# Performance work log

Hardware: AMD Instinct MI355X
Metric: run time of the kernel (lower is better)

Reference implementation:

```python
import jax, jax.numpy as jnp
import numpy as np

N_SETS, N_POINTS, D_FEAT = 8, 4096, 16
K = 16


def setup_inputs() -> dict:
    key = jax.random.key(0)
    x = jax.random.normal(key, (N_SETS, N_POINTS, D_FEAT), dtype=jnp.float32)
    return {"x": x, "k": K}


def reference(x, k):
    """Faithful kNN-graph construction.

    x: (N, M, D) point sets. Returns (src, dst) flattened edge lists with
    per-sample node-ID offsets (node j of set i -> global id i*M + j), plus
    the top-k squared distances (the selection values).
    """
    n_samples, n_points, _ = x.shape
    # pairwise squared distance: ||xi||^2 + ||xj||^2 - 2 xi.xj  -> (N, M, M)
    x2s = jnp.sum(x * x, axis=-1, keepdims=True)
    dist = x2s + jnp.swapaxes(x2s, -1, -2) - 2.0 * jnp.einsum("nmd,npd->nmp", x, x)
    # k smallest distances per row (argtopk descending=False)
    neg_vals, k_indices = jax.lax.top_k(-dist, k)            # (N, M, k)
    topk_dist = -neg_vals
    per_sample_offset = (jnp.arange(n_samples, dtype=jnp.int32) * n_points)[:, None, None]
    dst = k_indices.astype(jnp.int32) + per_sample_offset     # neighbor ids
    src = jnp.broadcast_to(
        jnp.arange(n_points, dtype=jnp.int32)[None, :, None], k_indices.shape
    ) + per_sample_offset                                     # query ids
    return src.reshape(-1), dst.reshape(-1), topk_dist
```

## Files before the change

### kernel.cpp

```cpp
#include <hip/hip_runtime.h>

typedef unsigned long long u64;

#define NSETS 8
#define NPTS  4096
#define DF    16
#define KNN   16
#define QPB   64
#define NCH   8
#define BLK   (QPB * NCH)
#define TILE  512
#define NTILE (NPTS / TILE)
#define SLICE (TILE / NCH)
#define NEDGE (NSETS * NPTS * KNN)

#define RES      10
#define FLUSH_AT 7
#define GRP      4

#define FEAT_B   (TILE * DF * 4)
#define NRM_B    (TILE * 4)
#define RESV_OFF (FEAT_B + NRM_B)
#define SMEM_B   (RESV_OFF + RES * BLK * 8)
#define MPAD     17

__device__ __forceinline__ unsigned flip_f(float d) {
    unsigned b = __float_as_uint(d);
    return (b & 0x80000000u) ? ~b : (b | 0x80000000u);
}
__device__ __forceinline__ float unflip_f(unsigned u) {
    unsigned b = (u & 0x80000000u) ? (u ^ 0x80000000u) : ~u;
    return __uint_as_float(b);
}

#define CEB(i, j) { u64 _a = B[i], _b = B[j]; bool _c = _b < _a; \
                    B[i] = _c ? _b : _a; B[j] = _c ? _a : _b; }
#define CEL(i, j) { u64 _a = Lk[i], _b = Lk[j]; bool _c = _b < _a; \
                    Lk[i] = _c ? _b : _a; Lk[j] = _c ? _a : _b; }
#define MERGE16() \
    CEL(0,8)  CEL(1,9)  CEL(2,10) CEL(3,11)  \
    CEL(4,12) CEL(5,13) CEL(6,14) CEL(7,15)  \
    CEL(0,4)  CEL(1,5)  CEL(2,6)  CEL(3,7)   \
    CEL(8,12) CEL(9,13) CEL(10,14) CEL(11,15) \
    CEL(0,2)  CEL(1,3)  CEL(4,6)  CEL(5,7)   \
    CEL(8,10) CEL(9,11) CEL(12,14) CEL(13,15) \
    CEL(0,1)  CEL(2,3)  CEL(4,5)  CEL(6,7)   \
    CEL(8,9)  CEL(10,11) CEL(12,13) CEL(14,15)

__global__ __launch_bounds__(BLK) void knn_kernel(const float* __restrict__ x,
                                                  float* __restrict__ out) {
    __shared__ float tau_sh[QPB];
    __shared__ float tau2_sh[NCH * QPB];
    __shared__ __align__(16) char smem[SMEM_B];
    float4* feat4 = (float4*)smem;
    float*  nrm_t = (float*)(smem + FEAT_B);
    u64*    resv  = (u64*)(smem + RESV_OFF);
    float*          lds_d = (float*)smem;
    unsigned short* lds_i = (unsigned short*)(smem + BLK * MPAD * 4);

    const int t    = threadIdx.x;
    const int lane = t & 63;
    const int wv   = t >> 6;
    const int set  = blockIdx.x >> 6;
    const int q0   = (blockIdx.x & 63) * QPB;
    const int q    = q0 + lane;

    const float* xs = x + (size_t)set * NPTS * DF;

    if (t < QPB) tau_sh[t] = 3.0e38f;
    tau2_sh[t] = 3.0e38f;

    float qn[DF];
    float q2;
    {
        const float4* qp = (const float4*)(xs + (size_t)q * DF);
        float4 a = qp[0], b = qp[1], g = qp[2], d = qp[3];
        float r0 = __fadd_rn(__fmul_rn(a.x, a.x), __fmul_rn(g.x, g.x));
        float r1 = __fadd_rn(__fmul_rn(a.y, a.y), __fmul_rn(g.y, g.y));
        float r2 = __fadd_rn(__fmul_rn(a.z, a.z), __fmul_rn(g.z, g.z));
        float r3 = __fadd_rn(__fmul_rn(a.w, a.w), __fmul_rn(g.w, g.w));
        float r4 = __fadd_rn(__fmul_rn(b.x, b.x), __fmul_rn(d.x, d.x));
        float r5 = __fadd_rn(__fmul_rn(b.y, b.y), __fmul_rn(d.y, d.y));
        float r6 = __fadd_rn(__fmul_rn(b.z, b.z), __fmul_rn(d.z, d.z));
        float r7 = __fadd_rn(__fmul_rn(b.w, b.w), __fmul_rn(d.w, d.w));
        q2 = __fadd_rn(__fadd_rn(__fadd_rn(r0, r1), __fadd_rn(r2, r3)),
                       __fadd_rn(__fadd_rn(r4, r5), __fadd_rn(r6, r7)));
        qn[0]=a.x; qn[1]=a.y; qn[2]=a.z; qn[3]=a.w;
        qn[4]=b.x; qn[5]=b.y; qn[6]=b.z; qn[7]=b.w;
        qn[8]=g.x; qn[9]=g.y; qn[10]=g.z; qn[11]=g.w;
        qn[12]=d.x; qn[13]=d.y; qn[14]=d.z; qn[15]=d.w;
#pragma unroll
        for (int d2 = 0; d2 < DF; ++d2) qn[d2] = -2.0f * qn[d2];
    }

    const u64 SENT = ((u64)flip_f(3.0e38f) << 32) | 0xFFFFFFFFull;
    u64   Lk[KNN];
#pragma unroll
    for (int j = 0; j < KNN; ++j) Lk[j] = SENT;
    float tau_reg = 3.0e38f;
    int   cnt = 0;

    auto drain = [&]() {
        {
            u64 B[8];
#pragma unroll
            for (int e = 0; e < 8; ++e) {
                u64 v = resv[e * BLK + t];
                B[e] = (e < cnt) ? v : SENT;
            }
            CEB(0,1) CEB(2,3) CEB(4,5) CEB(6,7)
            CEB(0,2) CEB(1,3) CEB(4,6) CEB(5,7)
            CEB(1,2) CEB(5,6)
            CEB(0,4) CEB(1,5) CEB(2,6) CEB(3,7)
            CEB(2,4) CEB(3,5)
            CEB(1,2) CEB(3,4) CEB(5,6)
#pragma unroll
            for (int i = 0; i < 8; ++i) {
                u64 a = Lk[KNN - 1 - i], b = B[i];
                Lk[KNN - 1 - i] = (b < a) ? b : a;
            }
            MERGE16()
        }
        if (__any(cnt > 8)) {
            u64 c0 = resv[8 * BLK + t];
            u64 c1 = resv[9 * BLK + t];
            c0 = (8 < cnt) ? c0 : SENT;
            c1 = (9 < cnt) ? c1 : SENT;
            { u64 a = c0, b = c1; bool c = b < a; c0 = c ? b : a; c1 = c ? a : b; }
            { u64 a = Lk[15]; Lk[15] = (c0 < a) ? c0 : a; }
            { u64 a = Lk[14]; Lk[14] = (c1 < a) ? c1 : a; }
            MERGE16()
        }
        cnt = 0;
        const float kth = unflip_f((unsigned)(Lk[KNN - 1] >> 32));
        volatile float* t2 = (volatile float*)tau2_sh;
        t2[wv * QPB + lane] = unflip_f((unsigned)(Lk[1] >> 32));
        float gmax = t2[0 * QPB + lane];
#pragma unroll
        for (int j = 1; j < NCH; ++j) gmax = fmaxf(gmax, t2[j * QPB + lane]);
        const float kth2 = fminf(kth, gmax);
        tau_reg = kth2;
        volatile float* ts = (volatile float*)tau_sh;
        float cur = ts[lane];
        ts[lane] = fminf(cur, kth2);
    };

    for (int tile = 0; tile < NTILE; ++tile) {
        __syncthreads();
        {
            const int c = tile * TILE + t;
            const float4* p = (const float4*)(xs + (size_t)c * DF);
            float4 a = p[0], b = p[1], g = p[2], d = p[3];
            float r0 = __fadd_rn(__fmul_rn(a.x, a.x), __fmul_rn(g.x, g.x));
            float r1 = __fadd_rn(__fmul_rn(a.y, a.y), __fmul_rn(g.y, g.y));
            float r2 = __fadd_rn(__fmul_rn(a.z, a.z), __fmul_rn(g.z, g.z));
            float r3 = __fadd_rn(__fmul_rn(a.w, a.w), __fmul_rn(g.w, g.w));
            float r4 = __fadd_rn(__fmul_rn(b.x, b.x), __fmul_rn(d.x, d.x));
            float r5 = __fadd_rn(__fmul_rn(b.y, b.y), __fmul_rn(d.y, d.y));
            float r6 = __fadd_rn(__fmul_rn(b.z, b.z), __fmul_rn(d.z, d.z));
            float r7 = __fadd_rn(__fmul_rn(b.w, b.w), __fmul_rn(d.w, d.w));
            feat4[0 * TILE + t] = a;
            feat4[1 * TILE + t] = b;
            feat4[2 * TILE + t] = g;
            feat4[3 * TILE + t] = d;
            nrm_t[t] = __fadd_rn(
                __fadd_rn(__fadd_rn(r0, r1), __fadd_rn(r2, r3)),
                __fadd_rn(__fadd_rn(r4, r5), __fadd_rn(r6, r7)));
        }
        __syncthreads();

        const int lbase = wv * SLICE;
        const int gbase = tile * TILE + lbase;

        for (int g = 0; g < SLICE; g += GRP) {
            const float tsh = ((volatile float*)tau_sh)[lane];
            const float tau = fminf(tsh, tau_reg);
#pragma unroll
            for (int u = 0; u < GRP; ++u) {
                const int lc = lbase + g + u;
                float4 f0 = feat4[0 * TILE + lc];
                float4 f1 = feat4[1 * TILE + lc];
                float4 f2 = feat4[2 * TILE + lc];
                float4 f3 = feat4[3 * TILE + lc];
                const float nc = nrm_t[lc];
                float dot = 0.f;
                dot = fmaf(qn[0],  f0.x, dot); dot = fmaf(qn[1],  f0.y, dot);
                dot = fmaf(qn[2],  f0.z, dot); dot = fmaf(qn[3],  f0.w, dot);
                dot = fmaf(qn[4],  f1.x, dot); dot = fmaf(qn[5],  f1.y, dot);
                dot = fmaf(qn[6],  f1.z, dot); dot = fmaf(qn[7],  f1.w, dot);
                dot = fmaf(qn[8],  f2.x, dot); dot = fmaf(qn[9],  f2.y, dot);
                dot = fmaf(qn[10], f2.z, dot); dot = fmaf(qn[11], f2.w, dot);
                dot = fmaf(qn[12], f3.x, dot); dot = fmaf(qn[13], f3.y, dot);
                dot = fmaf(qn[14], f3.z, dot); dot = fmaf(qn[15], f3.w, dot);
                const float dist = __fadd_rn(__fadd_rn(q2, nc), dot);
                if (dist <= tau) {
                    resv[cnt * BLK + t] =
                        ((u64)flip_f(dist) << 32) | (unsigned)(gbase + g + u);
                    ++cnt;
                }
            }
            if (__any(cnt >= FLUSH_AT)) drain();
        }
    }
    if (__any(cnt > 0)) drain();

    __syncthreads();
#pragma unroll
    for (int j = 0; j < KNN; ++j) {
        lds_d[t * MPAD + j] = unflip_f((unsigned)(Lk[j] >> 32));
        lds_i[t * MPAD + j] = (unsigned short)(Lk[j] & 0xFFFFu);
    }
    __syncthreads();

    if (t < QPB) {
        const int l = t;
        float h[NCH];
        int   hi[NCH];
        int   p[NCH];
#pragma unroll
        for (int w2 = 0; w2 < NCH; ++w2) {
            p[w2]  = 0;
            h[w2]  = lds_d[(w2 * QPB + l) * MPAD];
            hi[w2] = (int)lds_i[(w2 * QPB + l) * MPAD];
        }

        const int    gq = set * NPTS + q0 + l;
        const size_t eb = (size_t)gq * KNN;
        float* osrc = out;
        float* odst = out + (size_t)NEDGE;
        float* odis = out + 2 * (size_t)NEDGE;
        const float srcf = (float)gq;

        for (int e = 0; e < KNN; ++e) {
            float best = h[0];
            int   bi   = hi[0];
            int   bw   = 0;
#pragma unroll
            for (int w2 = 1; w2 < NCH; ++w2) {
                const bool better = (h[w2] < best) ||
                                    (h[w2] == best && hi[w2] < bi);
                if (better) { best = h[w2]; bi = hi[w2]; bw = w2; }
            }

#pragma unroll
            for (int w2 = 0; w2 < NCH; ++w2) {
                if (bw == w2) {
                    ++p[w2];
                    if (p[w2] < KNN) {
                        h[w2]  = lds_d[(w2 * QPB + l) * MPAD + p[w2]];
                        hi[w2] = (int)lds_i[(w2 * QPB + l) * MPAD + p[w2]];
                    } else {
                        h[w2]  = 3.0e38f;
                        hi[w2] = 0x7FFFFFFF;
                    }
                }
            }

            osrc[eb + e] = srcf;
            odst[eb + e] = (float)(set * NPTS + bi);
            odis[eb + e] = best;
        }
    }
}

extern "C" void kernel_launch(void* const* d_in, const int* in_sizes, int n_in,
                              void* d_out, int out_size, void* d_ws, size_t ws_size,
                              hipStream_t stream) {
    (void)in_sizes; (void)n_in; (void)out_size; (void)d_ws; (void)ws_size;
    const float* x = (const float*)d_in[0];
    float* out = (float*)d_out;

    knn_kernel<<<NSETS * (NPTS / QPB), BLK, 0, stream>>>(x, out);
}
```

Baseline: 199.8 us.

## Interleave candidate pairs in LDS for packed FP32 FMA and branchless reservoir writes

Candidate points are staged in shared memory as interleaved pairs, so each query computes two distances at once with 2-wide vector FMAs. On this hardware these can map to packed FP32 instructions, roughly halving the dot-product instruction count. Candidate norms are stored as two partial sums and added at use time, which slightly changes rounding order. The reservoir is split into separate distance and index arrays and filled branchlessly: every candidate is written and the count advances only when it passes the threshold, which removes divergent branches at the cost of extra LDS stores.

```diff
diff --git a/kernel.cpp b/kernel.cpp
--- a/kernel.cpp
+++ b/kernel.cpp
@@ -1,6 +1,9 @@
 #include <hip/hip_runtime.h>
 
 typedef unsigned long long u64;
+typedef unsigned int u32;
+typedef float f2 __attribute__((ext_vector_type(2)));
+typedef float f4 __attribute__((ext_vector_type(4)));
 
 #define NSETS 8
 #define NPTS  4096
@@ -12,15 +15,17 @@
 #define TILE  512
 #define NTILE (NPTS / TILE)
 #define SLICE (TILE / NCH)
+#define PAIRS_W (SLICE / 2)
 #define NEDGE (NSETS * NPTS * KNN)
 
 #define RES      10
 #define FLUSH_AT 7
-#define GRP      4
-
-#define FEAT_B   (TILE * DF * 4)
-#define NRM_B    (TILE * 4)
-#define RESV_OFF (FEAT_B + NRM_B)
+#define GRP      2
+
+#define PF_B     (TILE * DF * 4)
+#define PRT_OFF  PF_B
+#define RESV_OFF (PF_B + 4096)
+#define RESI_OFF (RESV_OFF + RES * BLK * 4)
 #define SMEM_B   (RESV_OFF + RES * BLK * 8)
 #define MPAD     17
 
@@ -31,6 +36,16 @@
 __device__ __forceinline__ float unflip_f(unsigned u) {
     unsigned b = (u & 0x80000000u) ? (u ^ 0x80000000u) : ~u;
     return __uint_as_float(b);
+}
+
+__device__ __forceinline__ f2 sp2(float v) { f2 r = {v, v}; return r; }
+
+__device__ __forceinline__ f2 fma2(f2 a, f2 b, f2 c) {
+#if __has_builtin(__builtin_elementwise_fma)
+    return __builtin_elementwise_fma(a, b, c);
+#else
+    f2 r; r.x = fmaf(a.x, b.x, c.x); r.y = fmaf(a.y, b.y, c.y); return r;
+#endif
 }
 
 #define CEB(i, j) { u64 _a = B[i], _b = B[j]; bool _c = _b < _a; \
@@ -52,9 +67,10 @@
     __shared__ float tau_sh[QPB];
     __shared__ float tau2_sh[NCH * QPB];
     __shared__ __align__(16) char smem[SMEM_B];
-    float4* feat4 = (float4*)smem;
-    float*  nrm_t = (float*)(smem + FEAT_B);
-    u64*    resv  = (u64*)(smem + RESV_OFF);
+    f4*    pf   = (f4*)smem;
+    f2*    prt  = (f2*)(smem + PRT_OFF);
+    float* resd = (float*)(smem + RESV_OFF);
+    u32*   resi = (u32*)(smem + RESI_OFF);
     float*          lds_d = (float*)smem;
     unsigned short* lds_i = (unsigned short*)(smem + BLK * MPAD * 4);
 
@@ -92,6 +108,7 @@
 #pragma unroll
         for (int d2 = 0; d2 < DF; ++d2) qn[d2] = -2.0f * qn[d2];
     }
+    const f2 q22 = sp2(q2);
 
     const u64 SENT = ((u64)flip_f(3.0e38f) << 32) | 0xFFFFFFFFull;
     u64   Lk[KNN];
@@ -105,8 +122,10 @@
             u64 B[8];
 #pragma unroll
             for (int e = 0; e < 8; ++e) {
-                u64 v = resv[e * BLK + t];
-                B[e] = (e < cnt) ? v : SENT;
+                float de = resd[e * BLK + t];
+                u32   ie = resi[e * BLK + t];
+                u64 key = ((u64)flip_f(de) << 32) | ie;
+                B[e] = (e < cnt) ? key : SENT;
             }
             CEB(0,1) CEB(2,3) CEB(4,5) CEB(6,7)
             CEB(0,2) CEB(1,3) CEB(4,6) CEB(5,7)
@@ -122,8 +141,10 @@
             MERGE16()
         }
         if (__any(cnt > 8)) {
-            u64 c0 = resv[8 * BLK + t];
-            u64 c1 = resv[9 * BLK + t];
+            float d8 = resd[8 * BLK + t], d9 = resd[9 * BLK + t];
+            u32   i8 = resi[8 * BLK + t], i9 = resi[9 * BLK + t];
+            u64 c0 = ((u64)flip_f(d8) << 32) | i8;
+            u64 c1 = ((u64)flip_f(d9) << 32) | i9;
             c0 = (8 < cnt) ? c0 : SENT;
             c1 = (9 < cnt) ? c1 : SENT;
             { u64 a = c0, b = c1; bool c = b < a; c0 = c ? b : a; c1 = c ? a : b; }
@@ -148,56 +169,78 @@
     for (int tile = 0; tile < NTILE; ++tile) {
         __syncthreads();
         {
-            const int c = tile * TILE + t;
-            const float4* p = (const float4*)(xs + (size_t)c * DF);
-            float4 a = p[0], b = p[1], g = p[2], d = p[3];
-            float r0 = __fadd_rn(__fmul_rn(a.x, a.x), __fmul_rn(g.x, g.x));
-            float r1 = __fadd_rn(__fmul_rn(a.y, a.y), __fmul_rn(g.y, g.y));
-            float r2 = __fadd_rn(__fmul_rn(a.z, a.z), __fmul_rn(g.z, g.z));
-            float r3 = __fadd_rn(__fmul_rn(a.w, a.w), __fmul_rn(g.w, g.w));
-            float r4 = __fadd_rn(__fmul_rn(b.x, b.x), __fmul_rn(d.x, d.x));
-            float r5 = __fadd_rn(__fmul_rn(b.y, b.y), __fmul_rn(d.y, d.y));
-            float r6 = __fadd_rn(__fmul_rn(b.z, b.z), __fmul_rn(d.z, d.z));
-            float r7 = __fadd_rn(__fmul_rn(b.w, b.w), __fmul_rn(d.w, d.w));
-            feat4[0 * TILE + t] = a;
-            feat4[1 * TILE + t] = b;
-            feat4[2 * TILE + t] = g;
-            feat4[3 * TILE + t] = d;
-            nrm_t[t] = __fadd_rn(
-                __fadd_rn(__fadd_rn(r0, r1), __fadd_rn(r2, r3)),
-                __fadd_rn(__fadd_rn(r4, r5), __fadd_rn(r6, r7)));
+            const int p  = t & 255;
+            const int hf = t >> 8;
+            const float4* rowA =
+                (const float4*)(xs + (size_t)(tile * TILE + 2 * p) * DF);
+            float4 a0 = rowA[hf];
+            float4 a2 = rowA[hf + 2];
+            float4 b0 = rowA[hf + 4];
+            float4 b2 = rowA[hf + 6];
+            const int jb0 = 2 * hf;
+            const int jb2 = 4 + 2 * hf;
+            pf[(jb0 + 0) * 256 + p] = (f4){a0.x, b0.x, a0.y, b0.y};
+            pf[(jb0 + 1) * 256 + p] = (f4){a0.z, b0.z, a0.w, b0.w};
+            pf[(jb2 + 0) * 256 + p] = (f4){a2.x, b2.x, a2.y, b2.y};
+            pf[(jb2 + 1) * 256 + p] = (f4){a2.z, b2.z, a2.w, b2.w};
+            float ra0 = __fadd_rn(__fmul_rn(a0.x, a0.x), __fmul_rn(a2.x, a2.x));
+            float ra1 = __fadd_rn(__fmul_rn(a0.y, a0.y), __fmul_rn(a2.y, a2.y));
+            float ra2 = __fadd_rn(__fmul_rn(a0.z, a0.z), __fmul_rn(a2.z, a2.z));
+            float ra3 = __fadd_rn(__fmul_rn(a0.w, a0.w), __fmul_rn(a2.w, a2.w));
+            float rb0 = __fadd_rn(__fmul_rn(b0.x, b0.x), __fmul_rn(b2.x, b2.x));
+            float rb1 = __fadd_rn(__fmul_rn(b0.y, b0.y), __fmul_rn(b2.y, b2.y));
+            float rb2 = __fadd_rn(__fmul_rn(b0.z, b0.z), __fmul_rn(b2.z, b2.z));
+            float rb3 = __fadd_rn(__fmul_rn(b0.w, b0.w), __fmul_rn(b2.w, b2.w));
+            f2 s;
+            s.x = __fadd_rn(__fadd_rn(ra0, ra1), __fadd_rn(ra2, ra3));
+            s.y = __fadd_rn(__fadd_rn(rb0, rb1), __fadd_rn(rb2, rb3));
+            prt[hf * 256 + p] = s;
         }
         __syncthreads();
 
-        const int lbase = wv * SLICE;
-        const int gbase = tile * TILE + lbase;
-
-        for (int g = 0; g < SLICE; g += GRP) {
+        const int pb = wv * PAIRS_W;
+
+        for (int g = 0; g < PAIRS_W; g += GRP) {
             const float tsh = ((volatile float*)tau_sh)[lane];
             const float tau = fminf(tsh, tau_reg);
 #pragma unroll
             for (int u = 0; u < GRP; ++u) {
-                const int lc = lbase + g + u;
-                float4 f0 = feat4[0 * TILE + lc];
-                float4 f1 = feat4[1 * TILE + lc];
-                float4 f2 = feat4[2 * TILE + lc];
-                float4 f3 = feat4[3 * TILE + lc];
-                const float nc = nrm_t[lc];
-                float dot = 0.f;
-                dot = fmaf(qn[0],  f0.x, dot); dot = fmaf(qn[1],  f0.y, dot);
-                dot = fmaf(qn[2],  f0.z, dot); dot = fmaf(qn[3],  f0.w, dot);
-                dot = fmaf(qn[4],  f1.x, dot); dot = fmaf(qn[5],  f1.y, dot);
-                dot = fmaf(qn[6],  f1.z, dot); dot = fmaf(qn[7],  f1.w, dot);
-                dot = fmaf(qn[8],  f2.x, dot); dot = fmaf(qn[9],  f2.y, dot);
-                dot = fmaf(qn[10], f2.z, dot); dot = fmaf(qn[11], f2.w, dot);
-                dot = fmaf(qn[12], f3.x, dot); dot = fmaf(qn[13], f3.y, dot);
-                dot = fmaf(qn[14], f3.z, dot); dot = fmaf(qn[15], f3.w, dot);
-                const float dist = __fadd_rn(__fadd_rn(q2, nc), dot);
-                if (dist <= tau) {
-                    resv[cnt * BLK + t] =
-                        ((u64)flip_f(dist) << 32) | (unsigned)(gbase + g + u);
-                    ++cnt;
-                }
+                const int lp = pb + g + u;
+                const f4* pp = pf + lp;
+                f4 c0 = pp[0 * 256];
+                f4 c1 = pp[1 * 256];
+                f4 c2 = pp[2 * 256];
+                f4 c3 = pp[3 * 256];
+                f4 c4 = pp[4 * 256];
+                f4 c5 = pp[5 * 256];
+                f4 c6 = pp[6 * 256];
+                f4 c7 = pp[7 * 256];
+                const f2 nn = prt[lp] + prt[256 + lp];
+                f2 acc = {0.f, 0.f};
+                acc = fma2(sp2(qn[0]),  c0.lo, acc);
+                acc = fma2(sp2(qn[1]),  c0.hi, acc);
+                acc = fma2(sp2(qn[2]),  c1.lo, acc);
+                acc = fma2(sp2(qn[3]),  c1.hi, acc);
+                acc = fma2(sp2(qn[4]),  c2.lo, acc);
+                acc = fma2(sp2(qn[5]),  c2.hi, acc);
+                acc = fma2(sp2(qn[6]),  c3.lo, acc);
+                acc = fma2(sp2(qn[7]),  c3.hi, acc);
+                acc = fma2(sp2(qn[8]),  c4.lo, acc);
+                acc = fma2(sp2(qn[9]),  c4.hi, acc);
+                acc = fma2(sp2(qn[10]), c5.lo, acc);
+                acc = fma2(sp2(qn[11]), c5.hi, acc);
+                acc = fma2(sp2(qn[12]), c6.lo, acc);
+                acc = fma2(sp2(qn[13]), c6.hi, acc);
+                acc = fma2(sp2(qn[14]), c7.lo, acc);
+                acc = fma2(sp2(qn[15]), c7.hi, acc);
+                const f2 dd = (q22 + nn) + acc;
+                const u32 gA = (u32)(tile * TILE + 2 * lp);
+                int sl = cnt * BLK + t;
+                resd[sl] = dd.x; resi[sl] = gA;
+                cnt += (dd.x <= tau) ? 1 : 0;
+                sl = cnt * BLK + t;
+                resd[sl] = dd.y; resi[sl] = gA + 1;
+                cnt += (dd.y <= tau) ? 1 : 0;
             }
             if (__any(cnt >= FLUSH_AT)) drain();
         }
```

Measured after the change: 260.0 us. 30.2% more time.
